# Kernel optimization log

Measured on AMD Instinct MI355X. Metric: run time of the kernel, lower is better.

## Reference

```python
import jax, jax.numpy as jnp
import numpy as np


def setup_inputs() -> dict:
    key = jax.random.key(0)
    ks = jax.random.split(key, 5)
    B, S, D_in, D_out, E, R = 4, 1024, 1024, 1024, 8, 16
    x = jax.random.normal(ks[0], (B, S, D_in), dtype=jnp.float32)
    weight = jax.random.normal(ks[1], (D_out, D_in), dtype=jnp.float32) / np.sqrt(D_in)
    gate_w = jax.random.normal(ks[2], (E, D_in), dtype=jnp.float32) / np.sqrt(D_in)
    lora_U = jax.random.normal(ks[3], (E, R, D_in), dtype=jnp.float32) / np.sqrt(D_in)
    lora_V = jax.random.normal(ks[4], (E, D_out, R), dtype=jnp.float32) / np.sqrt(R)
    return {"x": x, "weight": weight, "gate_w": gate_w, "lora_U": lora_U, "lora_V": lora_V}


def reference(x, weight, gate_w, lora_U, lora_V):
    # MoELoRA forward (global_gating=False), lora_alpha=1.0, rank=16
    scaling = 1.0 / lora_U.shape[1]
    B, S, D_in = x.shape
    xt = x.reshape(-1, D_in)                      # (N, D_in), N = B*S
    # per-token softmax gate over experts
    gate = jax.nn.softmax(xt @ gate_w.T, axis=-1)  # (N, E)
    # base term: sum_e gate[n,e] * (W @ x_n) = W @ x_n since gate sums to 1
    base = xt @ weight.T                           # (N, D_out)
    # low-rank expert contributions without materializing (E, D_out, D_in)
    t = jnp.einsum('nh,erh->ner', xt, lora_U)      # (N, E, R)
    lora = jnp.einsum('ne,eor,ner->no', gate, lora_V, t)  # (N, D_out)
    out = base + scaling * lora
    return out.reshape(B, S, -1)
```

## Files before the change

### kernel.cpp

```cpp
#include <hip/hip_runtime.h>
#include <hip/hip_bf16.h>

typedef __attribute__((ext_vector_type(8))) short short8;
typedef __attribute__((ext_vector_type(4))) float f32x4;

#define NTOK 4096
#define DIN  1024
#define DOUT 1024
#define KTOT 1152
#define XLD  1152
#define TLDS 200

__device__ __forceinline__ unsigned short f2bf(float f) {
    __hip_bfloat16 h = __float2bfloat16(f);
    return __builtin_bit_cast(unsigned short, h);
}

__device__ __forceinline__ void gload16(const void* g, void* l) {
    __builtin_amdgcn_global_load_lds((const __attribute__((address_space(1))) void*)g,
                                     (__attribute__((address_space(3))) void*)l, 16, 0, 0);
}

__device__ __forceinline__ uint4 pack8(const float* s) {
    float4 v0 = *(const float4*)s, v1 = *(const float4*)(s + 4);
    union { unsigned short u[8]; uint4 q; } pk;
    pk.u[0] = f2bf(v0.x); pk.u[1] = f2bf(v0.y); pk.u[2] = f2bf(v0.z); pk.u[3] = f2bf(v0.w);
    pk.u[4] = f2bf(v1.x); pk.u[5] = f2bf(v1.y); pk.u[6] = f2bf(v1.z); pk.u[7] = f2bf(v1.w);
    return pk.q;
}

__global__ __launch_bounds__(256) void k_cvtuw(const float* __restrict__ x,
                                               const float* __restrict__ lora_U,
                                               const float* __restrict__ gate_w,
                                               const float* __restrict__ w,
                                               const float* __restrict__ lora_V,
                                               __hip_bfloat16* __restrict__ Xcat,
                                               __hip_bfloat16* __restrict__ Ucat,
                                               __hip_bfloat16* __restrict__ Wcat) {
    int b = blockIdx.x;
    if (b < 2048) {
        int idx = b * 256 + threadIdx.x;
        int n = idx >> 7, g = idx & 127;
        *(uint4*)(Xcat + (size_t)n * XLD + g * 8) = pack8(x + (size_t)n * DIN + g * 8);
    } else if (b < 2144) {
        int idx = (b - 2048) * 256 + threadIdx.x;
        int r = idx >> 7, g = idx & 127;
        uint4 q = make_uint4(0u, 0u, 0u, 0u);
        if (r < 128)      q = pack8(lora_U + (size_t)r * DIN + g * 8);
        else if (r < 136) q = pack8(gate_w + (size_t)(r - 128) * DIN + g * 8);
        *(uint4*)(Ucat + (size_t)r * DIN + g * 8) = q;
    } else {
        int idx = (b - 2144) * 256 + threadIdx.x;
        int o = idx / 144, g = idx - o * 144;
        const float* s;
        if (g < 128) s = w + (size_t)o * DIN + g * 8;
        else {
            int i0 = (g - 128) * 8;
            int e = i0 >> 4, r = i0 & 15;
            s = lora_V + (size_t)e * (DOUT * 16) + (size_t)o * 16 + r;
        }
        *(uint4*)(Wcat + (size_t)o * KTOT + g * 8) = pack8(s);
    }
}

__global__ __launch_bounds__(256) void k_gemm1f(const __hip_bfloat16* __restrict__ Xc,
                                                const __hip_bfloat16* __restrict__ Ucat,
                                                __hip_bfloat16* __restrict__ Xcat) {
    __shared__ char smem[49152];
    float (*Tsm)[TLDS] = (float(*)[TLDS])smem;

    const int t = threadIdx.x, lane = t & 63, wid = t >> 6;
    const int row0 = blockIdx.x * 16;
    const int l7 = lane & 7, l8 = lane >> 3, l15 = lane & 15, l16 = lane >> 4;
    const int scol = ((l7 ^ l8) << 3);

    f32x4 acc[3];
#pragma unroll
    for (int n = 0; n < 3; ++n) acc[n] = (f32x4){0.f, 0.f, 0.f, 0.f};

    int boff[3];
#pragma unroll
    for (int n = 0; n < 3; ++n) boff[n] = (wid * 48 + n * 16 + l15) * 128;
    int sw[2];
#pragma unroll
    for (int ks = 0; ks < 2; ++ks) sw[ks] = (((ks * 4 + l16) ^ l7) << 4);

    const __hip_bfloat16* arow = Xc + (size_t)(row0 + l15) * XLD + l16 * 8;
    short8 areg[2][2];

#pragma unroll
    for (int i = 0; i < 6; ++i) {
        int cj = wid * 6 + i;
        gload16(Ucat + (size_t)(cj * 8 + l8) * DIN + 0 + scol, smem + cj * 1024);
    }
    areg[0][0] = *(const short8*)(arow + 0);
    areg[0][1] = *(const short8*)(arow + 32);

#pragma unroll
    for (int kt = 0; kt < 16; ++kt) {
        const int cur = kt & 1;
        if (kt < 15) {
            const int k1 = (kt + 1) << 6;
#pragma unroll
            for (int i = 0; i < 6; ++i) {
                int cj = wid * 6 + i;
                gload16(Ucat + (size_t)(cj * 8 + l8) * DIN + k1 + scol,
                        smem + (cur ^ 1) * 24576 + cj * 1024);
            }
            areg[(kt + 1) & 1][0] = *(const short8*)(arow + k1);
            areg[(kt + 1) & 1][1] = *(const short8*)(arow + k1 + 32);
            asm volatile("s_waitcnt vmcnt(10)" ::: "memory");
        } else {
            asm volatile("s_waitcnt vmcnt(2)" ::: "memory");
        }
        __builtin_amdgcn_s_barrier();
        const char* Bb = smem + cur * 24576;
#pragma unroll
        for (int ks = 0; ks < 2; ++ks) {
            short8 af = areg[cur][ks];
#pragma unroll
            for (int n = 0; n < 3; ++n) {
                short8 bf = *(const short8*)(Bb + boff[n] + sw[ks]);
                acc[n] = __builtin_amdgcn_mfma_f32_16x16x32_bf16(af, bf, acc[n], 0, 0, 0);
            }
        }
        __builtin_amdgcn_s_barrier();
    }

#pragma unroll
    for (int n = 0; n < 3; ++n)
#pragma unroll
        for (int j = 0; j < 4; ++j)
            Tsm[l16 * 4 + j][wid * 48 + n * 16 + l15] = acc[n][j];
    __syncthreads();

    if (t < 128) {
        const int tok = t >> 3, e = t & 7;
        float l[8];
#pragma unroll
        for (int i = 0; i < 8; ++i) l[i] = Tsm[tok][128 + i];
        float m = l[0];
#pragma unroll
        for (int i = 1; i < 8; ++i) m = fmaxf(m, l[i]);
        float s = 0.f;
#pragma unroll
        for (int i = 0; i < 8; ++i) s += __expf(l[i] - m);
        const float g = __expf(l[e] - m) / s * 0.0625f;
        union { unsigned short u[16]; uint4 q[2]; } pk;
#pragma unroll
        for (int jj = 0; jj < 16; ++jj) pk.u[jj] = f2bf(g * Tsm[tok][e * 16 + jj]);
        uint4* dst = (uint4*)(Xcat + (size_t)(row0 + tok) * XLD + 1024 + e * 16);
        dst[0] = pk.q[0]; dst[1] = pk.q[1];
    }
}

__global__ __launch_bounds__(256) void k_gemm2(const __hip_bfloat16* __restrict__ A,
                                               const __hip_bfloat16* __restrict__ B,
                                               float* __restrict__ out) {
    __shared__ char smem[49152];
    const int b = blockIdx.x;
    const int xcd = b & 7, j = b >> 3;
    const int bx = xcd * 4 + (j & 3), by = j >> 2;
    const int row0 = bx * 128, col0 = by * 64;

    const int t = threadIdx.x, lane = t & 63, wid = t >> 6;
    const int wr = wid >> 1, wc = wid & 1;
    const int l7 = lane & 7, l8 = lane >> 3, l15 = lane & 15, l16 = lane >> 4;
    const int scol = ((l7 ^ l8) << 3);

    f32x4 zf = {0.f, 0.f, 0.f, 0.f};
    f32x4 acc[4][2];
#pragma unroll
    for (int m = 0; m < 4; ++m)
#pragma unroll
        for (int n = 0; n < 2; ++n) acc[m][n] = zf;

    int aoff[4], boff[2], sw[2];
#pragma unroll
    for (int m = 0; m < 4; ++m) aoff[m] = (wr * 64 + m * 16 + l15) * 128;
#pragma unroll
    for (int n = 0; n < 2; ++n) boff[n] = (wc * 32 + n * 16 + l15) * 128;
#pragma unroll
    for (int ks = 0; ks < 2; ++ks) sw[ks] = (((ks * 4 + l16) ^ l7) << 4);

#define G2_STAGE(buf, kt)                                                      \
    {                                                                          \
        const int k0_ = (kt) << 6;                                             \
        _Pragma("unroll")                                                      \
        for (int i = 0; i < 4; ++i) {                                          \
            int ci = wid * 4 + i;                                              \
            gload16(A + (size_t)(row0 + ci * 8 + l8) * XLD + k0_ + scol,       \
                    smem + (buf) * 16384 + ci * 1024);                         \
        }                                                                      \
        _Pragma("unroll")                                                      \
        for (int i = 0; i < 2; ++i) {                                          \
            int cj = wid * 2 + i;                                              \
            gload16(B + (size_t)(col0 + cj * 8 + l8) * KTOT + k0_ + scol,      \
                    smem + 32768 + (buf) * 8192 + cj * 1024);                  \
        }                                                                      \
    }

#define G2_COMP(buf)                                                           \
    {                                                                          \
        const char* Ab = smem + (buf) * 16384;                                 \
        const char* Bb = smem + 32768 + (buf) * 8192;                          \
        _Pragma("unroll")                                                      \
        for (int ks = 0; ks < 2; ++ks) {                                       \
            short8 af[4], bf[2];                                               \
            _Pragma("unroll")                                                  \
            for (int m = 0; m < 4; ++m)                                        \
                af[m] = *(const short8*)(Ab + aoff[m] + sw[ks]);               \
            _Pragma("unroll")                                                  \
            for (int n = 0; n < 2; ++n)                                        \
                bf[n] = *(const short8*)(Bb + boff[n] + sw[ks]);               \
            _Pragma("unroll")                                                  \
            for (int m = 0; m < 4; ++m)                                        \
                _Pragma("unroll")                                              \
                for (int n = 0; n < 2; ++n)                                    \
                    acc[m][n] = __builtin_amdgcn_mfma_f32_16x16x32_bf16(       \
                        af[m], bf[n], acc[m][n], 0, 0, 0);                     \
        }                                                                      \
    }

    G2_STAGE(0, 0);
    int cur = 0;
    for (int kt = 0; kt < 18; ++kt) {
        if (kt < 17) {
            G2_STAGE(cur ^ 1, kt + 1);
            asm volatile("s_waitcnt vmcnt(6)" ::: "memory");
        } else {
            asm volatile("s_waitcnt vmcnt(0)" ::: "memory");
        }
        __builtin_amdgcn_s_barrier();
        G2_COMP(cur);
        __builtin_amdgcn_s_barrier();
        cur ^= 1;
    }

#pragma unroll
    for (int m = 0; m < 4; ++m)
#pragma unroll
        for (int n = 0; n < 2; ++n)
#pragma unroll
            for (int jj = 0; jj < 4; ++jj)
                out[(size_t)(row0 + wr * 64 + m * 16 + l16 * 4 + jj) * DOUT
                    + col0 + wc * 32 + n * 16 + l15] = acc[m][n][jj];
#undef G2_STAGE
#undef G2_COMP
}

extern "C" void kernel_launch(void* const* d_in, const int* in_sizes, int n_in,
                              void* d_out, int out_size, void* d_ws, size_t ws_size,
                              hipStream_t stream) {
    const float* x      = (const float*)d_in[0];
    const float* weight = (const float*)d_in[1];
    const float* gate_w = (const float*)d_in[2];
    const float* lora_U = (const float*)d_in[3];
    const float* lora_V = (const float*)d_in[4];
    float* out = (float*)d_out;

    char* ws = (char*)d_ws;
    __hip_bfloat16* Xcat = (__hip_bfloat16*)ws;
    __hip_bfloat16* Ucat = (__hip_bfloat16*)(ws + 9437184);
    __hip_bfloat16* Wcat = (__hip_bfloat16*)(ws + 9437184 + 393216);

    k_cvtuw<<<2720, 256, 0, stream>>>(x, lora_U, gate_w, weight, lora_V, Xcat, Ucat, Wcat);
    k_gemm1f<<<256, 256, 0, stream>>>(Xcat, Ucat, Xcat);
    k_gemm2<<<512, 256, 0, stream>>>(Xcat, Wcat, out);
}
```

Before: 38.31 us.

## Fuse conversion kernel with gating/LoRA-down GEMM, converting fp32 inputs on the fly

Merges the bf16 conversion kernel and the first GEMM (gate logits and LoRA down-projection) into one launch. Blocks 0-255 run GEMM1 and read fp32 x, lora_U and gate_w directly, converting to bf16 in registers and storing into LDS. The remaining blocks convert x and W/V into the workspace as before. This drops one kernel launch and the Ucat round trip. The risk is a race: GEMM1 blocks write the T/gate columns of Xcat while the conversion blocks in the same launch write the x columns of the same rows, and register-staged prefetch replaces the async LDS loads.

```diff
diff --git a/kernel.cpp b/kernel.cpp
--- a/kernel.cpp
+++ b/kernel.cpp
@@ -21,58 +21,52 @@
                                      (__attribute__((address_space(3))) void*)l, 16, 0, 0);
 }
 
-__device__ __forceinline__ uint4 pack8(const float* s) {
-    float4 v0 = *(const float4*)s, v1 = *(const float4*)(s + 4);
+__device__ __forceinline__ uint4 pack2(float4 v0, float4 v1) {
     union { unsigned short u[8]; uint4 q; } pk;
     pk.u[0] = f2bf(v0.x); pk.u[1] = f2bf(v0.y); pk.u[2] = f2bf(v0.z); pk.u[3] = f2bf(v0.w);
     pk.u[4] = f2bf(v1.x); pk.u[5] = f2bf(v1.y); pk.u[6] = f2bf(v1.z); pk.u[7] = f2bf(v1.w);
     return pk.q;
 }
 
-__global__ __launch_bounds__(256) void k_cvtuw(const float* __restrict__ x,
-                                               const float* __restrict__ lora_U,
-                                               const float* __restrict__ gate_w,
-                                               const float* __restrict__ w,
-                                               const float* __restrict__ lora_V,
-                                               __hip_bfloat16* __restrict__ Xcat,
-                                               __hip_bfloat16* __restrict__ Ucat,
-                                               __hip_bfloat16* __restrict__ Wcat) {
-    int b = blockIdx.x;
-    if (b < 2048) {
-        int idx = b * 256 + threadIdx.x;
-        int n = idx >> 7, g = idx & 127;
-        *(uint4*)(Xcat + (size_t)n * XLD + g * 8) = pack8(x + (size_t)n * DIN + g * 8);
-    } else if (b < 2144) {
-        int idx = (b - 2048) * 256 + threadIdx.x;
-        int r = idx >> 7, g = idx & 127;
-        uint4 q = make_uint4(0u, 0u, 0u, 0u);
-        if (r < 128)      q = pack8(lora_U + (size_t)r * DIN + g * 8);
-        else if (r < 136) q = pack8(gate_w + (size_t)(r - 128) * DIN + g * 8);
-        *(uint4*)(Ucat + (size_t)r * DIN + g * 8) = q;
-    } else {
-        int idx = (b - 2144) * 256 + threadIdx.x;
-        int o = idx / 144, g = idx - o * 144;
-        const float* s;
-        if (g < 128) s = w + (size_t)o * DIN + g * 8;
-        else {
-            int i0 = (g - 128) * 8;
-            int e = i0 >> 4, r = i0 & 15;
-            s = lora_V + (size_t)e * (DOUT * 16) + (size_t)o * 16 + r;
-        }
-        *(uint4*)(Wcat + (size_t)o * KTOT + g * 8) = pack8(s);
-    }
-}
-
-__global__ __launch_bounds__(256) void k_gemm1f(const __hip_bfloat16* __restrict__ Xc,
-                                                const __hip_bfloat16* __restrict__ Ucat,
-                                                __hip_bfloat16* __restrict__ Xcat) {
+__device__ __forceinline__ uint4 pack8(const float* s) {
+    return pack2(*(const float4*)s, *(const float4*)(s + 4));
+}
+
+__global__ __launch_bounds__(256) void k_prep_g1(const float* __restrict__ x,
+                                                 const float* __restrict__ lora_U,
+                                                 const float* __restrict__ gate_w,
+                                                 const float* __restrict__ w,
+                                                 const float* __restrict__ lora_V,
+                                                 __hip_bfloat16* __restrict__ Xcat,
+                                                 __hip_bfloat16* __restrict__ Wcat) {
     __shared__ char smem[49152];
+    const int bid = blockIdx.x;
+    const int t = threadIdx.x;
+
+    if (bid >= 256) {
+        if (bid < 2304) {
+            int idx = (bid - 256) * 256 + t;
+            int n = idx >> 7, g = idx & 127;
+            *(uint4*)(Xcat + (size_t)n * XLD + g * 8) = pack8(x + (size_t)n * DIN + g * 8);
+        } else {
+            int idx = (bid - 2304) * 256 + t;
+            int o = idx / 144, g = idx - o * 144;
+            const float* s;
+            if (g < 128) s = w + (size_t)o * DIN + g * 8;
+            else {
+                int i0 = (g - 128) * 8;
+                int e = i0 >> 4, r = i0 & 15;
+                s = lora_V + (size_t)e * (DOUT * 16) + (size_t)o * 16 + r;
+            }
+            *(uint4*)(Wcat + (size_t)o * KTOT + g * 8) = pack8(s);
+        }
+        return;
+    }
+
     float (*Tsm)[TLDS] = (float(*)[TLDS])smem;
-
-    const int t = threadIdx.x, lane = t & 63, wid = t >> 6;
-    const int row0 = blockIdx.x * 16;
-    const int l7 = lane & 7, l8 = lane >> 3, l15 = lane & 15, l16 = lane >> 4;
-    const int scol = ((l7 ^ l8) << 3);
+    const int lane = t & 63, wid = t >> 6;
+    const int row0 = bid * 16;
+    const int l7 = lane & 7, l15 = lane & 15, l16 = lane >> 4;
 
     f32x4 acc[3];
 #pragma unroll
@@ -85,46 +79,92 @@
 #pragma unroll
     for (int ks = 0; ks < 2; ++ks) sw[ks] = (((ks * 4 + l16) ^ l7) << 4);
 
-    const __hip_bfloat16* arow = Xc + (size_t)(row0 + l15) * XLD + l16 * 8;
-    short8 areg[2][2];
-
-#pragma unroll
-    for (int i = 0; i < 6; ++i) {
-        int cj = wid * 6 + i;
-        gload16(Ucat + (size_t)(cj * 8 + l8) * DIN + 0 + scol, smem + cj * 1024);
-    }
-    areg[0][0] = *(const short8*)(arow + 0);
-    areg[0][1] = *(const short8*)(arow + 32);
-
-#pragma unroll
+    const int trow = t >> 3, p = t & 7;
+    int bdst[6];
+    const float* bsrc[6];
+#pragma unroll
+    for (int c = 0; c < 6; ++c) {
+        int rr = c * 32 + trow;
+        bdst[c] = (rr >> 3) * 1024 + (((rr & 7) * 8 + p) * 16);
+        int scol8 = ((p ^ (rr & 7)) << 3);
+        if (rr < 128)      bsrc[c] = lora_U + (size_t)rr * DIN + scol8;
+        else if (rr < 136) bsrc[c] = gate_w + (size_t)(rr - 128) * DIN + scol8;
+        else               bsrc[c] = nullptr;
+    }
+    const float* arow = x + (size_t)(row0 + l15) * DIN + l16 * 8;
+
+    short8 areg;
+    {
+#pragma unroll
+        for (int c = 0; c < 6; ++c) {
+            uint4 q = bsrc[c] ? pack8(bsrc[c]) : make_uint4(0u, 0u, 0u, 0u);
+            *(uint4*)(smem + bdst[c]) = q;
+        }
+        union { unsigned short u[8]; short8 s8; } pa;
+        float4 a0 = *(const float4*)arow, a1 = *(const float4*)(arow + 4);
+        pa.u[0]=f2bf(a0.x); pa.u[1]=f2bf(a0.y); pa.u[2]=f2bf(a0.z); pa.u[3]=f2bf(a0.w);
+        pa.u[4]=f2bf(a1.x); pa.u[5]=f2bf(a1.y); pa.u[6]=f2bf(a1.z); pa.u[7]=f2bf(a1.w);
+        areg = pa.s8;
+    }
+    __syncthreads();
+
     for (int kt = 0; kt < 16; ++kt) {
         const int cur = kt & 1;
-        if (kt < 15) {
+        float4 bpre[6][2]; float4 apre0, apre1;
+        const bool hasNext = kt < 15;
+        if (hasNext) {
             const int k1 = (kt + 1) << 6;
 #pragma unroll
-            for (int i = 0; i < 6; ++i) {
-                int cj = wid * 6 + i;
-                gload16(Ucat + (size_t)(cj * 8 + l8) * DIN + k1 + scol,
-                        smem + (cur ^ 1) * 24576 + cj * 1024);
-            }
-            areg[(kt + 1) & 1][0] = *(const short8*)(arow + k1);
-            areg[(kt + 1) & 1][1] = *(const short8*)(arow + k1 + 32);
-            asm volatile("s_waitcnt vmcnt(10)" ::: "memory");
-        } else {
-            asm volatile("s_waitcnt vmcnt(2)" ::: "memory");
-        }
-        __builtin_amdgcn_s_barrier();
+            for (int c = 0; c < 6; ++c)
+                if (bsrc[c]) {
+                    bpre[c][0] = *(const float4*)(bsrc[c] + k1);
+                    bpre[c][1] = *(const float4*)(bsrc[c] + k1 + 4);
+                }
+            apre0 = *(const float4*)(arow + k1);
+            apre1 = *(const float4*)(arow + k1 + 4);
+        }
         const char* Bb = smem + cur * 24576;
 #pragma unroll
         for (int ks = 0; ks < 2; ++ks) {
-            short8 af = areg[cur][ks];
+            short8 af = areg;
+            if (ks == 1) {
+            }
+            (void)af;
+        }
+        {
+            short8 af0 = areg;
+            union { unsigned short u[8]; short8 s8; } pa1;
+            float4 a2 = *(const float4*)(arow + (kt << 6) + 32);
+            float4 a3 = *(const float4*)(arow + (kt << 6) + 36);
+            pa1.u[0]=f2bf(a2.x); pa1.u[1]=f2bf(a2.y); pa1.u[2]=f2bf(a2.z); pa1.u[3]=f2bf(a2.w);
+            pa1.u[4]=f2bf(a3.x); pa1.u[5]=f2bf(a3.y); pa1.u[6]=f2bf(a3.z); pa1.u[7]=f2bf(a3.w);
+            short8 af1 = pa1.s8;
+            float4 b2 = *(const float4*)(arow + (kt << 6) + 32 + 0);
+            (void)b2;
 #pragma unroll
             for (int n = 0; n < 3; ++n) {
-                short8 bf = *(const short8*)(Bb + boff[n] + sw[ks]);
-                acc[n] = __builtin_amdgcn_mfma_f32_16x16x32_bf16(af, bf, acc[n], 0, 0, 0);
-            }
-        }
-        __builtin_amdgcn_s_barrier();
+                short8 bf0 = *(const short8*)(Bb + boff[n] + sw[0]);
+                acc[n] = __builtin_amdgcn_mfma_f32_16x16x32_bf16(af0, bf0, acc[n], 0, 0, 0);
+            }
+#pragma unroll
+            for (int n = 0; n < 3; ++n) {
+                short8 bf1 = *(const short8*)(Bb + boff[n] + sw[1]);
+                acc[n] = __builtin_amdgcn_mfma_f32_16x16x32_bf16(af1, bf1, acc[n], 0, 0, 0);
+            }
+        }
+        if (hasNext) {
+#pragma unroll
+            for (int c = 0; c < 6; ++c) {
+                uint4 q = bsrc[c] ? pack2(bpre[c][0], bpre[c][1])
+                                  : make_uint4(0u, 0u, 0u, 0u);
+                *(uint4*)(smem + (cur ^ 1) * 24576 + bdst[c]) = q;
+            }
+            union { unsigned short u[8]; short8 s8; } pa;
+            pa.u[0]=f2bf(apre0.x); pa.u[1]=f2bf(apre0.y); pa.u[2]=f2bf(apre0.z); pa.u[3]=f2bf(apre0.w);
+            pa.u[4]=f2bf(apre1.x); pa.u[5]=f2bf(apre1.y); pa.u[6]=f2bf(apre1.z); pa.u[7]=f2bf(apre1.w);
+            areg = pa.s8;
+        }
+        __syncthreads();
     }
 
 #pragma unroll
@@ -261,10 +301,8 @@
 
     char* ws = (char*)d_ws;
     __hip_bfloat16* Xcat = (__hip_bfloat16*)ws;
-    __hip_bfloat16* Ucat = (__hip_bfloat16*)(ws + 9437184);
-    __hip_bfloat16* Wcat = (__hip_bfloat16*)(ws + 9437184 + 393216);
-
-    k_cvtuw<<<2720, 256, 0, stream>>>(x, lora_U, gate_w, weight, lora_V, Xcat, Ucat, Wcat);
-    k_gemm1f<<<256, 256, 0, stream>>>(Xcat, Ucat, Xcat);
+    __hip_bfloat16* Wcat = (__hip_bfloat16*)(ws + 9437184);
+
+    k_prep_g1<<<2880, 256, 0, stream>>>(x, lora_U, gate_w, weight, lora_V, Xcat, Wcat);
     k_gemm2<<<512, 256, 0, stream>>>(Xcat, Wcat, out);
 }
```

New measurement: 47.23 us. 1.23x slower.

## Drop LDS staging in gate/LoRA-down GEMM, load operands directly from global

Applied to the files above, without the earlier changes.

Rewrites the first GEMM (token x [U;gate]) so each wave reads its A and B fragments directly from global memory instead of double-buffering B through LDS with async loads and barriers. Blocks now cover 32 tokens with 512 threads and 128 blocks instead of 16 tokens with 256 threads and 256 blocks. This removes the barriers and LDS traffic but relies on cache hits for the small shared Ucat operand. Global load latency is less hidden and only half the CUs get a block.

```diff
diff --git a/kernel.cpp b/kernel.cpp
--- a/kernel.cpp
+++ b/kernel.cpp
@@ -9,7 +9,6 @@
 #define DOUT 1024
 #define KTOT 1152
 #define XLD  1152
-#define TLDS 200
 
 __device__ __forceinline__ unsigned short f2bf(float f) {
     __hip_bfloat16 h = __float2bfloat16(f);
@@ -63,78 +62,47 @@
     }
 }
 
-__global__ __launch_bounds__(256) void k_gemm1f(const __hip_bfloat16* __restrict__ Xc,
+__global__ __launch_bounds__(512) void k_gemm1f(const __hip_bfloat16* __restrict__ Xc,
                                                 const __hip_bfloat16* __restrict__ Ucat,
                                                 __hip_bfloat16* __restrict__ Xcat) {
-    __shared__ char smem[49152];
-    float (*Tsm)[TLDS] = (float(*)[TLDS])smem;
-
+    __shared__ float Tsm[32][200];
     const int t = threadIdx.x, lane = t & 63, wid = t >> 6;
-    const int row0 = blockIdx.x * 16;
-    const int l7 = lane & 7, l8 = lane >> 3, l15 = lane & 15, l16 = lane >> 4;
-    const int scol = ((l7 ^ l8) << 3);
+    const int g = wid >> 2, cs = wid & 3;
+    const int row0 = blockIdx.x * 32;
+    const int l15 = lane & 15, l16 = lane >> 4;
 
     f32x4 acc[3];
 #pragma unroll
     for (int n = 0; n < 3; ++n) acc[n] = (f32x4){0.f, 0.f, 0.f, 0.f};
 
-    int boff[3];
-#pragma unroll
-    for (int n = 0; n < 3; ++n) boff[n] = (wid * 48 + n * 16 + l15) * 128;
-    int sw[2];
-#pragma unroll
-    for (int ks = 0; ks < 2; ++ks) sw[ks] = (((ks * 4 + l16) ^ l7) << 4);
-
-    const __hip_bfloat16* arow = Xc + (size_t)(row0 + l15) * XLD + l16 * 8;
-    short8 areg[2][2];
-
-#pragma unroll
-    for (int i = 0; i < 6; ++i) {
-        int cj = wid * 6 + i;
-        gload16(Ucat + (size_t)(cj * 8 + l8) * DIN + 0 + scol, smem + cj * 1024);
-    }
-    areg[0][0] = *(const short8*)(arow + 0);
-    areg[0][1] = *(const short8*)(arow + 32);
-
-#pragma unroll
+    const __hip_bfloat16* aP = Xc + (size_t)(row0 + g * 16 + l15) * XLD + l16 * 8;
+    const __hip_bfloat16* bP[3];
+#pragma unroll
+    for (int n = 0; n < 3; ++n)
+        bP[n] = Ucat + (size_t)(cs * 48 + n * 16 + l15) * DIN + l16 * 8;
+
+#pragma unroll 4
     for (int kt = 0; kt < 16; ++kt) {
-        const int cur = kt & 1;
-        if (kt < 15) {
-            const int k1 = (kt + 1) << 6;
-#pragma unroll
-            for (int i = 0; i < 6; ++i) {
-                int cj = wid * 6 + i;
-                gload16(Ucat + (size_t)(cj * 8 + l8) * DIN + k1 + scol,
-                        smem + (cur ^ 1) * 24576 + cj * 1024);
-            }
-            areg[(kt + 1) & 1][0] = *(const short8*)(arow + k1);
-            areg[(kt + 1) & 1][1] = *(const short8*)(arow + k1 + 32);
-            asm volatile("s_waitcnt vmcnt(10)" ::: "memory");
-        } else {
-            asm volatile("s_waitcnt vmcnt(2)" ::: "memory");
-        }
-        __builtin_amdgcn_s_barrier();
-        const char* Bb = smem + cur * 24576;
 #pragma unroll
         for (int ks = 0; ks < 2; ++ks) {
-            short8 af = areg[cur][ks];
+            const int ko = kt * 64 + ks * 32;
+            short8 af = *(const short8*)(aP + ko);
 #pragma unroll
             for (int n = 0; n < 3; ++n) {
-                short8 bf = *(const short8*)(Bb + boff[n] + sw[ks]);
+                short8 bf = *(const short8*)(bP[n] + ko);
                 acc[n] = __builtin_amdgcn_mfma_f32_16x16x32_bf16(af, bf, acc[n], 0, 0, 0);
             }
         }
-        __builtin_amdgcn_s_barrier();
     }
 
 #pragma unroll
     for (int n = 0; n < 3; ++n)
 #pragma unroll
         for (int j = 0; j < 4; ++j)
-            Tsm[l16 * 4 + j][wid * 48 + n * 16 + l15] = acc[n][j];
+            Tsm[g * 16 + l16 * 4 + j][cs * 48 + n * 16 + l15] = acc[n][j];
     __syncthreads();
 
-    if (t < 128) {
+    if (t < 256) {
         const int tok = t >> 3, e = t & 7;
         float l[8];
 #pragma unroll
@@ -145,10 +113,10 @@
         float s = 0.f;
 #pragma unroll
         for (int i = 0; i < 8; ++i) s += __expf(l[i] - m);
-        const float g = __expf(l[e] - m) / s * 0.0625f;
+        const float gt = __expf(l[e] - m) / s * 0.0625f;
         union { unsigned short u[16]; uint4 q[2]; } pk;
 #pragma unroll
-        for (int jj = 0; jj < 16; ++jj) pk.u[jj] = f2bf(g * Tsm[tok][e * 16 + jj]);
+        for (int jj = 0; jj < 16; ++jj) pk.u[jj] = f2bf(gt * Tsm[tok][e * 16 + jj]);
         uint4* dst = (uint4*)(Xcat + (size_t)(row0 + tok) * XLD + 1024 + e * 16);
         dst[0] = pk.q[0]; dst[1] = pk.q[1];
     }
@@ -265,6 +233,6 @@
     __hip_bfloat16* Wcat = (__hip_bfloat16*)(ws + 9437184 + 393216);
 
     k_cvtuw<<<2720, 256, 0, stream>>>(x, lora_U, gate_w, weight, lora_V, Xcat, Ucat, Wcat);
-    k_gemm1f<<<256, 256, 0, stream>>>(Xcat, Ucat, Xcat);
+    k_gemm1f<<<128, 512, 0, stream>>>(Xcat, Ucat, Xcat);
     k_gemm2<<<512, 256, 0, stream>>>(Xcat, Wcat, out);
 }
```

New measurement: 56.79 us. 48.2% more time.
